# Performance work log

Measured on AMD Instinct MI355X. Metric: run time of the kernel, lower is better.

The kernel has to match this reference:

```python
import jax, jax.numpy as jnp
import numpy as np

H = 16  # n_heads

def setup_inputs() -> dict:
    key = jax.random.key(0)
    ks = jax.random.split(key, 7)
    B, L, D = 4, 2048, 1024
    s = 0.02
    return {
        "z": jax.random.normal(ks[0], (B, L, D), jnp.float32),
        "connection": jax.random.normal(ks[1], (B, L, D), jnp.float32),
        "Wq": jax.random.normal(ks[2], (2 * D, D), jnp.float32) * s,
        "Wk": jax.random.normal(ks[3], (2 * D, D), jnp.float32) * s,
        "Wv": jax.random.normal(ks[4], (D, D), jnp.float32) * s,
        "Wo": jax.random.normal(ks[5], (D, D), jnp.float32) * s,
        "temp": jnp.float32(1.0),
    }

def reference(z, connection, Wq, Wk, Wv, Wo, temp):
    B, L, D = z.shape
    hd = D // H
    zc = jnp.concatenate([z, connection], axis=-1)          # [B,L,2D]
    Q = (zc @ Wq).reshape(B, L, H, hd).transpose(0, 2, 1, 3)  # [B,H,L,hd]
    K = (zc @ Wk).reshape(B, L, H, hd).transpose(0, 2, 1, 3)
    V = (z @ Wv).reshape(B, L, H, hd).transpose(0, 2, 1, 3)
    scale = (hd ** -0.5) * temp
    scores = jnp.einsum('bhqd,bhkd->bhqk', Q, K) * scale     # [B,H,L,L]
    rel = jax.nn.sigmoid(scores)
    rel_sum = jnp.clip(rel.sum(-1, keepdims=True), 1.0, None)
    out = jnp.einsum('bhqk,bhkd->bhqd', rel, V) / rel_sum
    out = out.transpose(0, 2, 1, 3).reshape(B, L, D)
    return out @ Wo
```

## Files before the change

kernel.cpp:

```cpp
#include <hip/hip_runtime.h>

typedef unsigned short u16;
typedef unsigned int u32;
typedef __bf16 bf16x8 __attribute__((ext_vector_type(8)));
typedef float f32x4 __attribute__((ext_vector_type(4)));

#define DEV static __device__ __forceinline__

DEV void gload16(const void* g, void* l) {
    __builtin_amdgcn_global_load_lds(
        (const __attribute__((address_space(1))) void*)g,
        (__attribute__((address_space(3))) void*)l, 16, 0, 0);
}

DEV void store_c(float* p, float v) { *p = v; }
DEV void store_c(u16* p, float v) { *(__bf16*)p = (__bf16)v; }

DEV int swz(int row, int bytecol) { return row * 128 + (bytecol ^ ((row & 7) << 4)); }
DEV int swzP(int row, int bytecol) {
    return row * 128 + (bytecol ^ ((row & 7) << 4) ^ (row & 8));
}

DEV void xcd_remap(int& bx, int& by, int gx, int gy) {
    int nwg = gx * gy;
    int bid = by * gx + bx;
    int logical = (bid & 7) * (nwg >> 3) + (bid >> 3);
    bx = logical % gx;
    by = logical / gx;
}

__global__ void pack_zc(const float* __restrict__ z, const float* __restrict__ cn,
                        u16* __restrict__ zc) {
    size_t i = ((size_t)blockIdx.x * blockDim.x + threadIdx.x) * 4;
    size_t t = i >> 11;
    int c = (int)(i & 2047);
    const float* src = (c < 1024) ? (z + t * 1024 + c) : (cn + t * 1024 + (c - 1024));
    float4 v = *reinterpret_cast<const float4*>(src);
    union { __bf16 h[4]; uint2 u; } o;
    o.h[0] = (__bf16)v.x; o.h[1] = (__bf16)v.y;
    o.h[2] = (__bf16)v.z; o.h[3] = (__bf16)v.w;
    *reinterpret_cast<uint2*>(zc + i) = o.u;
}

__global__ void transpose_conv_w(const float* __restrict__ W, u16* __restrict__ WT,
                                 int K, int N) {
    __shared__ float tile[32][33];
    int n0 = blockIdx.x * 32, k0 = blockIdx.y * 32;
    int tx = threadIdx.x, ty = threadIdx.y;
    #pragma unroll
    for (int i = ty; i < 32; i += 8)
        tile[i][tx] = W[(size_t)(k0 + i) * N + n0 + tx];
    __syncthreads();
    #pragma unroll
    for (int i = ty; i < 32; i += 8)
        *(__bf16*)&WT[(size_t)(n0 + i) * K + k0 + tx] = (__bf16)tile[tx][i];
}

__global__ void transpose_v(const u16* __restrict__ Vf, u16* __restrict__ Vt) {
    __shared__ u16 tile[32][33];
    int bh = blockIdx.z; int b = bh >> 4, h = bh & 15;
    int l0 = blockIdx.x * 32, d0 = blockIdx.y * 32;
    int tx = threadIdx.x, ty = threadIdx.y;
    #pragma unroll
    for (int i = ty; i < 32; i += 8)
        tile[i][tx] = Vf[(size_t)(b * 2048 + l0 + i) * 1024 + h * 64 + d0 + tx];
    __syncthreads();
    #pragma unroll
    for (int i = ty; i < 32; i += 8)
        Vt[((size_t)bh * 64 + d0 + i) * 2048 + l0 + tx] = tile[tx][i];
}

template <typename OutT>
__global__ __launch_bounds__(256, 2)
void gemm_bt(const u16* __restrict__ A, const u16* __restrict__ BT,
             OutT* __restrict__ C, int M, int N, int K,
             int lda, int ldb, int ldc) {
    __shared__ u16 As[128 * 64];
    __shared__ u16 Bs[128 * 64];
    const int tid = threadIdx.x;
    const int lane = tid & 63;
    const int wid = tid >> 6;
    int bx = blockIdx.x, by = blockIdx.y;
    xcd_remap(bx, by, gridDim.x, gridDim.y);
    const int m0 = bx * 128;
    const int n0 = by * 128;
    const int wr = (wid >> 1) * 64;
    const int wc = (wid & 1) * 64;

    f32x4 acc[4][4];
    #pragma unroll
    for (int i = 0; i < 4; ++i)
        #pragma unroll
        for (int j = 0; j < 4; ++j)
            acc[i][j] = f32x4{0.f, 0.f, 0.f, 0.f};

    const int srcoff = ((lane & 7) ^ (lane >> 3)) * 8;
    const int rb = wid * 32 + (lane >> 3);
    const u16* aptr[4]; const u16* bptr[4];
    #pragma unroll
    for (int p = 0; p < 4; ++p) {
        aptr[p] = A  + (size_t)(m0 + rb + p * 8) * lda + srcoff;
        bptr[p] = BT + (size_t)(n0 + rb + p * 8) * ldb + srcoff;
    }

    for (int k0 = 0; k0 < K; k0 += 64) {
        __syncthreads();
        #pragma unroll
        for (int p = 0; p < 4; ++p)
            gload16(aptr[p] + k0, (char*)As + (wid * 4 + p) * 1024);
        #pragma unroll
        for (int p = 0; p < 4; ++p)
            gload16(bptr[p] + k0, (char*)Bs + (wid * 4 + p) * 1024);
        __syncthreads();

        #pragma unroll
        for (int kk = 0; kk < 64; kk += 32) {
            bf16x8 af[4], bfr[4];
            #pragma unroll
            for (int i = 0; i < 4; ++i) {
                int row = wr + i * 16 + (lane & 15);
                af[i] = *reinterpret_cast<const bf16x8*>(
                    reinterpret_cast<const char*>(As) + swz(row, (kk + (lane >> 4) * 8) * 2));
            }
            #pragma unroll
            for (int j = 0; j < 4; ++j) {
                int row = wc + j * 16 + (lane & 15);
                bfr[j] = *reinterpret_cast<const bf16x8*>(
                    reinterpret_cast<const char*>(Bs) + swz(row, (kk + (lane >> 4) * 8) * 2));
            }
            #pragma unroll
            for (int i = 0; i < 4; ++i)
                #pragma unroll
                for (int j = 0; j < 4; ++j)
                    acc[i][j] = __builtin_amdgcn_mfma_f32_16x16x32_bf16(af[i], bfr[j], acc[i][j], 0, 0, 0);
        }
    }

    #pragma unroll
    for (int i = 0; i < 4; ++i)
        #pragma unroll
        for (int j = 0; j < 4; ++j)
            #pragma unroll
            for (int r = 0; r < 4; ++r) {
                int row = m0 + wr + i * 16 + (lane >> 4) * 4 + r;
                int col = n0 + wc + j * 16 + (lane & 15);
                store_c(&C[(size_t)row * ldc + col], acc[i][j][r]);
            }
}

__global__ __launch_bounds__(256, 2)
void attn_kernel(const u16* __restrict__ QKf, const u16* __restrict__ Vt,
                 u16* __restrict__ Oa, const float* __restrict__ temp) {
    constexpr int L = 2048, D = 1024, QKLD = 2048, HD = 64;
    __shared__ u16 Ks[2][64 * 64];
    __shared__ u16 Vs[2][64 * 64];
    __shared__ u16 Ps[4][32 * 64];

    const int tid = threadIdx.x;
    const int lane = tid & 63;
    const int wid = tid >> 6;
    const int hi = lane >> 4;
    int bx = blockIdx.x, by = blockIdx.y;
    xcd_remap(bx, by, gridDim.x, gridDim.y);
    const int bh = by;
    const int b = bh >> 4, h = bh & 15;
    const int q0 = bx * 128;
    const float sneg = -temp[0] * 0.125f * 1.44269504f;

    const u16* Qbase = QKf + (size_t)(b * L) * QKLD + h * HD;
    const u16* Kbase = Qbase + 1024;
    const u16* Vbase = Vt + (size_t)bh * HD * L;

    const int srcoff = ((lane & 7) ^ (lane >> 3)) * 8;
    const int rb = wid * 16 + (lane >> 3);
    const u16* kptr[2]; const u16* vptr[2];
    #pragma unroll
    for (int p = 0; p < 2; ++p) {
        kptr[p] = Kbase + (size_t)(rb + p * 8) * QKLD + srcoff;
        vptr[p] = Vbase + (size_t)(rb + p * 8) * L + srcoff;
    }

    bf16x8 qf[2][2];
    #pragma unroll
    for (int i = 0; i < 2; ++i)
        #pragma unroll
        for (int kx = 0; kx < 2; ++kx)
            qf[i][kx] = *reinterpret_cast<const bf16x8*>(
                Qbase + (size_t)(q0 + wid * 32 + i * 16 + (lane & 15)) * QKLD + kx * 32 + hi * 8);

    #pragma unroll
    for (int p = 0; p < 2; ++p)
        gload16(kptr[p], (char*)Ks[0] + (wid * 2 + p) * 1024);
    #pragma unroll
    for (int p = 0; p < 2; ++p)
        gload16(vptr[p], (char*)Vs[0] + (wid * 2 + p) * 1024);

    bf16x8 onesf;
    #pragma unroll
    for (int j = 0; j < 8; ++j) onesf[j] = (__bf16)1.0f;

    f32x4 oacc[4][2];
    #pragma unroll
    for (int ct = 0; ct < 4; ++ct)
        #pragma unroll
        for (int i = 0; i < 2; ++i) oacc[ct][i] = f32x4{0.f, 0.f, 0.f, 0.f};
    f32x4 racc[2];
    racc[0] = f32x4{0.f, 0.f, 0.f, 0.f};
    racc[1] = f32x4{0.f, 0.f, 0.f, 0.f};

    __syncthreads();
    int cur = 0;

    for (int k0 = 0; k0 < L; k0 += 64) {
        if (k0 + 64 < L) {
            #pragma unroll
            for (int p = 0; p < 2; ++p)
                gload16(kptr[p] + (size_t)(k0 + 64) * QKLD, (char*)Ks[cur ^ 1] + (wid * 2 + p) * 1024);
            #pragma unroll
            for (int p = 0; p < 2; ++p)
                gload16(vptr[p] + (k0 + 64), (char*)Vs[cur ^ 1] + (wid * 2 + p) * 1024);
        }

        f32x4 s[4][2];
        #pragma unroll
        for (int ct = 0; ct < 4; ++ct)
            #pragma unroll
            for (int i = 0; i < 2; ++i) s[ct][i] = f32x4{0.f, 0.f, 0.f, 0.f};
        #pragma unroll
        for (int kx = 0; kx < 2; ++kx) {
            bf16x8 ak[4];
            #pragma unroll
            for (int ct = 0; ct < 4; ++ct) {
                int krow = ct * 16 + (lane & 15);
                ak[ct] = *reinterpret_cast<const bf16x8*>(
                    reinterpret_cast<const char*>(Ks[cur]) + swz(krow, kx * 64 + hi * 16));
            }
            #pragma unroll
            for (int ct = 0; ct < 4; ++ct)
                #pragma unroll
                for (int i = 0; i < 2; ++i)
                    s[ct][i] = __builtin_amdgcn_mfma_f32_16x16x32_bf16(ak[ct], qf[i][kx], s[ct][i], 0, 0, 0);
        }

        #pragma unroll
        for (int i = 0; i < 2; ++i) {
            int prow = i * 16 + (lane & 15);
            #pragma unroll
            for (int ct = 0; ct < 4; ++ct) {
                union { __bf16 hh[4]; uint2 uu; } pk;
                #pragma unroll
                for (int r = 0; r < 4; ++r)
                    pk.hh[r] = (__bf16)__builtin_amdgcn_rcpf(1.0f + exp2f(s[ct][i][r] * sneg));
                *reinterpret_cast<uint2*>(reinterpret_cast<char*>(Ps[wid]) +
                    swzP(prow, ct * 32 + hi * 8)) = pk.uu;
            }
        }

        #pragma unroll
        for (int kx = 0; kx < 2; ++kx) {
            bf16x8 ap[2];
            #pragma unroll
            for (int i = 0; i < 2; ++i) {
                int prow = i * 16 + (lane & 15);
                union { u32 w[4]; bf16x8 v; } apu;
                *reinterpret_cast<uint2*>(&apu.w[0]) = *reinterpret_cast<const uint2*>(
                    reinterpret_cast<const char*>(Ps[wid]) + swzP(prow, kx * 64 + hi * 16));
                *reinterpret_cast<uint2*>(&apu.w[2]) = *reinterpret_cast<const uint2*>(
                    reinterpret_cast<const char*>(Ps[wid]) + swzP(prow, kx * 64 + hi * 16 + 8));
                ap[i] = apu.v;
            }
            racc[0] = __builtin_amdgcn_mfma_f32_16x16x32_bf16(ap[0], onesf, racc[0], 0, 0, 0);
            racc[1] = __builtin_amdgcn_mfma_f32_16x16x32_bf16(ap[1], onesf, racc[1], 0, 0, 0);
            #pragma unroll
            for (int ct = 0; ct < 4; ++ct) {
                int vrow = ct * 16 + (lane & 15);
                bf16x8 bv = *reinterpret_cast<const bf16x8*>(
                    reinterpret_cast<const char*>(Vs[cur]) + swz(vrow, kx * 64 + hi * 16));
                #pragma unroll
                for (int i = 0; i < 2; ++i)
                    oacc[ct][i] = __builtin_amdgcn_mfma_f32_16x16x32_bf16(ap[i], bv, oacc[ct][i], 0, 0, 0);
            }
        }

        __syncthreads();
        cur ^= 1;
    }

    float rdiv[2][4];
    #pragma unroll
    for (int i = 0; i < 2; ++i)
        #pragma unroll
        for (int r = 0; r < 4; ++r)
            rdiv[i][r] = __builtin_amdgcn_rcpf(fmaxf(racc[i][r], 1.0f));

    #pragma unroll
    for (int ct = 0; ct < 4; ++ct)
        #pragma unroll
        for (int i = 0; i < 2; ++i)
            #pragma unroll
            for (int r = 0; r < 4; ++r) {
                int row = q0 + wid * 32 + i * 16 + hi * 4 + r;
                int col = h * HD + ct * 16 + (lane & 15);
                *(__bf16*)&Oa[(size_t)(b * L + row) * D + col] =
                    (__bf16)(oacc[ct][i][r] * rdiv[i][r]);
            }
}

extern "C" void kernel_launch(void* const* d_in, const int* in_sizes, int n_in,
                              void* d_out, int out_size, void* d_ws, size_t ws_size,
                              hipStream_t stream) {
    const float* z    = (const float*)d_in[0];
    const float* cn   = (const float*)d_in[1];
    const float* Wq   = (const float*)d_in[2];
    const float* Wk   = (const float*)d_in[3];
    const float* Wv   = (const float*)d_in[4];
    const float* Wo   = (const float*)d_in[5];
    const float* temp = (const float*)d_in[6];

    char* ws = (char*)d_ws;
    u16* zc  = (u16*)ws; ws += (size_t)8192 * 2048 * 2;
    u16* WqT = (u16*)ws; ws += (size_t)1024 * 2048 * 2;
    u16* WkT = (u16*)ws; ws += (size_t)1024 * 2048 * 2;
    u16* WvT = (u16*)ws; ws += (size_t)1024 * 1024 * 2;
    u16* WoT = (u16*)ws; ws += (size_t)1024 * 1024 * 2;
    u16* QKf = (u16*)ws; ws += (size_t)8192 * 2048 * 2;
    u16* Vf  = (u16*)ws; ws += (size_t)8192 * 1024 * 2;
    u16* Vt  = zc;
    u16* Oa  = Vf;

    pack_zc<<<16384, 256, 0, stream>>>(z, cn, zc);

    dim3 tb(32, 8);
    transpose_conv_w<<<dim3(32, 64), tb, 0, stream>>>(Wq, WqT, 2048, 1024);
    transpose_conv_w<<<dim3(32, 64), tb, 0, stream>>>(Wk, WkT, 2048, 1024);
    transpose_conv_w<<<dim3(32, 32), tb, 0, stream>>>(Wv, WvT, 1024, 1024);
    transpose_conv_w<<<dim3(32, 32), tb, 0, stream>>>(Wo, WoT, 1024, 1024);

    gemm_bt<u16><<<dim3(64, 16), 256, 0, stream>>>(zc, WqT, QKf, 8192, 2048, 2048, 2048, 2048, 2048);
    gemm_bt<u16><<<dim3(64, 8),  256, 0, stream>>>(zc, WvT, Vf,  8192, 1024, 1024, 2048, 1024, 1024);

    transpose_v<<<dim3(64, 2, 64), tb, 0, stream>>>(Vf, Vt);

    attn_kernel<<<dim3(16, 64), 256, 0, stream>>>(QKf, Vt, Oa, temp);

    gemm_bt<float><<<dim3(64, 8), 256, 0, stream>>>(Oa, WoT, (float*)d_out, 8192, 1024, 1024, 1024, 1024, 1024);
}
```

Before: 410.4 us.

## Fuse V transpose into GEMM epilogue, fold scale into Wq, drop LDS staging

The V projection GEMM now writes its output directly in the transposed per-head layout, which removes the separate transpose_v kernel and its round trip through memory. The attention scale and log2(e) factor are folded into the bf16 conversion of Wq, so the sigmoid uses a raw exp2 on the scores with no extra multiply. The attention kernel also drops its double-buffered LDS staging of K and V and reads MFMA operands straight from global memory, removing the barriers. In exchange, K/V reuse across waves now relies on the cache instead of LDS, and the transposed stores are 8-byte scattered writes.

Result: slower. 527.2 us (+28.4%).

```diff
diff --git a/kernel.cpp b/kernel.cpp
--- a/kernel.cpp
+++ b/kernel.cpp
@@ -43,8 +43,9 @@
 }
 
 __global__ void transpose_conv_w(const float* __restrict__ W, u16* __restrict__ WT,
-                                 int K, int N) {
+                                 int K, int N, const float* __restrict__ scl) {
     __shared__ float tile[32][33];
+    float sc = scl ? scl[0] * 0.18033688011112042f : 1.0f;
     int n0 = blockIdx.x * 32, k0 = blockIdx.y * 32;
     int tx = threadIdx.x, ty = threadIdx.y;
     #pragma unroll
@@ -53,24 +54,10 @@
     __syncthreads();
     #pragma unroll
     for (int i = ty; i < 32; i += 8)
-        *(__bf16*)&WT[(size_t)(n0 + i) * K + k0 + tx] = (__bf16)tile[tx][i];
-}
-
-__global__ void transpose_v(const u16* __restrict__ Vf, u16* __restrict__ Vt) {
-    __shared__ u16 tile[32][33];
-    int bh = blockIdx.z; int b = bh >> 4, h = bh & 15;
-    int l0 = blockIdx.x * 32, d0 = blockIdx.y * 32;
-    int tx = threadIdx.x, ty = threadIdx.y;
-    #pragma unroll
-    for (int i = ty; i < 32; i += 8)
-        tile[i][tx] = Vf[(size_t)(b * 2048 + l0 + i) * 1024 + h * 64 + d0 + tx];
-    __syncthreads();
-    #pragma unroll
-    for (int i = ty; i < 32; i += 8)
-        Vt[((size_t)bh * 64 + d0 + i) * 2048 + l0 + tx] = tile[tx][i];
-}
-
-template <typename OutT>
+        *(__bf16*)&WT[(size_t)(n0 + i) * K + k0 + tx] = (__bf16)(tile[tx][i] * sc);
+}
+
+template <typename OutT, bool VT_OUT = false>
 __global__ __launch_bounds__(256, 2)
 void gemm_bt(const u16* __restrict__ A, const u16* __restrict__ BT,
              OutT* __restrict__ C, int M, int N, int K,
@@ -136,49 +123,58 @@
         }
     }
 
-    #pragma unroll
-    for (int i = 0; i < 4; ++i)
-        #pragma unroll
-        for (int j = 0; j < 4; ++j)
-            #pragma unroll
-            for (int r = 0; r < 4; ++r) {
-                int row = m0 + wr + i * 16 + (lane >> 4) * 4 + r;
-                int col = n0 + wc + j * 16 + (lane & 15);
-                store_c(&C[(size_t)row * ldc + col], acc[i][j][r]);
-            }
+    if constexpr (VT_OUT) {
+        #pragma unroll
+        for (int i = 0; i < 4; ++i)
+            #pragma unroll
+            for (int j = 0; j < 4; ++j) {
+                int row0 = m0 + wr + i * 16 + (lane >> 4) * 4;
+                int col  = n0 + wc + j * 16 + (lane & 15);
+                int b = row0 >> 11, l = row0 & 2047;
+                int h = col >> 6, hd = col & 63;
+                union { __bf16 hh[4]; uint2 uu; } o;
+                #pragma unroll
+                for (int r = 0; r < 4; ++r) o.hh[r] = (__bf16)acc[i][j][r];
+                *reinterpret_cast<uint2*>(
+                    (u16*)C + (((size_t)(b * 16 + h) * 64 + hd) * 2048 + l)) = o.uu;
+            }
+    } else {
+        #pragma unroll
+        for (int i = 0; i < 4; ++i)
+            #pragma unroll
+            for (int j = 0; j < 4; ++j)
+                #pragma unroll
+                for (int r = 0; r < 4; ++r) {
+                    int row = m0 + wr + i * 16 + (lane >> 4) * 4 + r;
+                    int col = n0 + wc + j * 16 + (lane & 15);
+                    store_c(&C[(size_t)row * ldc + col], acc[i][j][r]);
+                }
+    }
 }
 
 __global__ __launch_bounds__(256, 2)
 void attn_kernel(const u16* __restrict__ QKf, const u16* __restrict__ Vt,
-                 u16* __restrict__ Oa, const float* __restrict__ temp) {
+                 u16* __restrict__ Oa) {
     constexpr int L = 2048, D = 1024, QKLD = 2048, HD = 64;
-    __shared__ u16 Ks[2][64 * 64];
-    __shared__ u16 Vs[2][64 * 64];
     __shared__ u16 Ps[4][32 * 64];
 
     const int tid = threadIdx.x;
     const int lane = tid & 63;
     const int wid = tid >> 6;
     const int hi = lane >> 4;
+    const int lq = lane & 15;
     int bx = blockIdx.x, by = blockIdx.y;
     xcd_remap(bx, by, gridDim.x, gridDim.y);
     const int bh = by;
     const int b = bh >> 4, h = bh & 15;
     const int q0 = bx * 128;
-    const float sneg = -temp[0] * 0.125f * 1.44269504f;
 
     const u16* Qbase = QKf + (size_t)(b * L) * QKLD + h * HD;
     const u16* Kbase = Qbase + 1024;
     const u16* Vbase = Vt + (size_t)bh * HD * L;
 
-    const int srcoff = ((lane & 7) ^ (lane >> 3)) * 8;
-    const int rb = wid * 16 + (lane >> 3);
-    const u16* kptr[2]; const u16* vptr[2];
-    #pragma unroll
-    for (int p = 0; p < 2; ++p) {
-        kptr[p] = Kbase + (size_t)(rb + p * 8) * QKLD + srcoff;
-        vptr[p] = Vbase + (size_t)(rb + p * 8) * L + srcoff;
-    }
+    const u16* Kl = Kbase + (size_t)lq * QKLD + hi * 8;
+    const u16* Vl = Vbase + (size_t)lq * L + hi * 8;
 
     bf16x8 qf[2][2];
     #pragma unroll
@@ -186,14 +182,7 @@
         #pragma unroll
         for (int kx = 0; kx < 2; ++kx)
             qf[i][kx] = *reinterpret_cast<const bf16x8*>(
-                Qbase + (size_t)(q0 + wid * 32 + i * 16 + (lane & 15)) * QKLD + kx * 32 + hi * 8);
-
-    #pragma unroll
-    for (int p = 0; p < 2; ++p)
-        gload16(kptr[p], (char*)Ks[0] + (wid * 2 + p) * 1024);
-    #pragma unroll
-    for (int p = 0; p < 2; ++p)
-        gload16(vptr[p], (char*)Vs[0] + (wid * 2 + p) * 1024);
+                Qbase + (size_t)(q0 + wid * 32 + i * 16 + lq) * QKLD + kx * 32 + hi * 8);
 
     bf16x8 onesf;
     #pragma unroll
@@ -208,19 +197,7 @@
     racc[0] = f32x4{0.f, 0.f, 0.f, 0.f};
     racc[1] = f32x4{0.f, 0.f, 0.f, 0.f};
 
-    __syncthreads();
-    int cur = 0;
-
     for (int k0 = 0; k0 < L; k0 += 64) {
-        if (k0 + 64 < L) {
-            #pragma unroll
-            for (int p = 0; p < 2; ++p)
-                gload16(kptr[p] + (size_t)(k0 + 64) * QKLD, (char*)Ks[cur ^ 1] + (wid * 2 + p) * 1024);
-            #pragma unroll
-            for (int p = 0; p < 2; ++p)
-                gload16(vptr[p] + (k0 + 64), (char*)Vs[cur ^ 1] + (wid * 2 + p) * 1024);
-        }
-
         f32x4 s[4][2];
         #pragma unroll
         for (int ct = 0; ct < 4; ++ct)
@@ -230,11 +207,9 @@
         for (int kx = 0; kx < 2; ++kx) {
             bf16x8 ak[4];
             #pragma unroll
-            for (int ct = 0; ct < 4; ++ct) {
-                int krow = ct * 16 + (lane & 15);
+            for (int ct = 0; ct < 4; ++ct)
                 ak[ct] = *reinterpret_cast<const bf16x8*>(
-                    reinterpret_cast<const char*>(Ks[cur]) + swz(krow, kx * 64 + hi * 16));
-            }
+                    Kl + (size_t)(k0 + ct * 16) * QKLD + kx * 32);
             #pragma unroll
             for (int ct = 0; ct < 4; ++ct)
                 #pragma unroll
@@ -244,13 +219,14 @@
 
         #pragma unroll
         for (int i = 0; i < 2; ++i) {
-            int prow = i * 16 + (lane & 15);
+            int prow = i * 16 + lq;
             #pragma unroll
             for (int ct = 0; ct < 4; ++ct) {
                 union { __bf16 hh[4]; uint2 uu; } pk;
                 #pragma unroll
                 for (int r = 0; r < 4; ++r)
-                    pk.hh[r] = (__bf16)__builtin_amdgcn_rcpf(1.0f + exp2f(s[ct][i][r] * sneg));
+                    pk.hh[r] = (__bf16)__builtin_amdgcn_rcpf(
+                        1.0f + __builtin_amdgcn_exp2f(-s[ct][i][r]));
                 *reinterpret_cast<uint2*>(reinterpret_cast<char*>(Ps[wid]) +
                     swzP(prow, ct * 32 + hi * 8)) = pk.uu;
             }
@@ -261,7 +237,7 @@
             bf16x8 ap[2];
             #pragma unroll
             for (int i = 0; i < 2; ++i) {
-                int prow = i * 16 + (lane & 15);
+                int prow = i * 16 + lq;
                 union { u32 w[4]; bf16x8 v; } apu;
                 *reinterpret_cast<uint2*>(&apu.w[0]) = *reinterpret_cast<const uint2*>(
                     reinterpret_cast<const char*>(Ps[wid]) + swzP(prow, kx * 64 + hi * 16));
@@ -273,17 +249,13 @@
             racc[1] = __builtin_amdgcn_mfma_f32_16x16x32_bf16(ap[1], onesf, racc[1], 0, 0, 0);
             #pragma unroll
             for (int ct = 0; ct < 4; ++ct) {
-                int vrow = ct * 16 + (lane & 15);
                 bf16x8 bv = *reinterpret_cast<const bf16x8*>(
-                    reinterpret_cast<const char*>(Vs[cur]) + swz(vrow, kx * 64 + hi * 16));
+                    Vl + (size_t)(ct * 16) * L + k0 + kx * 32);
                 #pragma unroll
                 for (int i = 0; i < 2; ++i)
                     oacc[ct][i] = __builtin_amdgcn_mfma_f32_16x16x32_bf16(ap[i], bv, oacc[ct][i], 0, 0, 0);
             }
         }
-
-        __syncthreads();
-        cur ^= 1;
     }
 
     float rdiv[2][4];
@@ -300,7 +272,7 @@
             #pragma unroll
             for (int r = 0; r < 4; ++r) {
                 int row = q0 + wid * 32 + i * 16 + hi * 4 + r;
-                int col = h * HD + ct * 16 + (lane & 15);
+                int col = h * HD + ct * 16 + lq;
                 *(__bf16*)&Oa[(size_t)(b * L + row) * D + col] =
                     (__bf16)(oacc[ct][i][r] * rdiv[i][r]);
             }
@@ -324,24 +296,21 @@
     u16* WvT = (u16*)ws; ws += (size_t)1024 * 1024 * 2;
     u16* WoT = (u16*)ws; ws += (size_t)1024 * 1024 * 2;
     u16* QKf = (u16*)ws; ws += (size_t)8192 * 2048 * 2;
-    u16* Vf  = (u16*)ws; ws += (size_t)8192 * 1024 * 2;
-    u16* Vt  = zc;
-    u16* Oa  = Vf;
+    u16* Vt  = (u16*)ws; ws += (size_t)8192 * 1024 * 2;
+    u16* Oa  = zc;
 
     pack_zc<<<16384, 256, 0, stream>>>(z, cn, zc);
 
     dim3 tb(32, 8);
-    transpose_conv_w<<<dim3(32, 64), tb, 0, stream>>>(Wq, WqT, 2048, 1024);
-    transpose_conv_w<<<dim3(32, 64), tb, 0, stream>>>(Wk, WkT, 2048, 1024);
-    transpose_conv_w<<<dim3(32, 32), tb, 0, stream>>>(Wv, WvT, 1024, 1024);
-    transpose_conv_w<<<dim3(32, 32), tb, 0, stream>>>(Wo, WoT, 1024, 1024);
+    transpose_conv_w<<<dim3(32, 64), tb, 0, stream>>>(Wq, WqT, 2048, 1024, temp);
+    transpose_conv_w<<<dim3(32, 64), tb, 0, stream>>>(Wk, WkT, 2048, 1024, nullptr);
+    transpose_conv_w<<<dim3(32, 32), tb, 0, stream>>>(Wv, WvT, 1024, 1024, nullptr);
+    transpose_conv_w<<<dim3(32, 32), tb, 0, stream>>>(Wo, WoT, 1024, 1024, nullptr);
 
     gemm_bt<u16><<<dim3(64, 16), 256, 0, stream>>>(zc, WqT, QKf, 8192, 2048, 2048, 2048, 2048, 2048);
-    gemm_bt<u16><<<dim3(64, 8),  256, 0, stream>>>(zc, WvT, Vf,  8192, 1024, 1024, 2048, 1024, 1024);
-
-    transpose_v<<<dim3(64, 2, 64), tb, 0, stream>>>(Vf, Vt);
-
-    attn_kernel<<<dim3(16, 64), 256, 0, stream>>>(QKf, Vt, Oa, temp);
+    gemm_bt<u16, true><<<dim3(64, 8), 256, 0, stream>>>(zc, WvT, Vt, 8192, 1024, 1024, 2048, 1024, 0);
+
+    attn_kernel<<<dim3(16, 64), 256, 0, stream>>>(QKf, Vt, Oa);
 
     gemm_bt<float><<<dim3(64, 8), 256, 0, stream>>>(Oa, WoT, (float*)d_out, 8192, 1024, 1024, 1024, 1024, 1024);
 }
```
